# Kernel optimization log

Measured on AMD Instinct MI355X. Metric: run time of the kernel, lower is better.

Reference implementation:

```python
import jax, jax.numpy as jnp
import numpy as np

N, E, D, H = 100000, 200000, 384, 768
BN_EPS = 1e-5


def setup_inputs() -> dict:
    key = jax.random.key(0)
    ks = jax.random.split(key, 8)
    w = lambda k, sh: jax.random.normal(k, sh, jnp.float32) * 0.02
    return {
        "x": jax.random.normal(ks[0], (N, D), jnp.float32),
        "edge_attr": jax.random.normal(ks[1], (E, D), jnp.float32),
        "gamma": jnp.ones((D,), jnp.float32),
        "beta": jnp.zeros((D,), jnp.float32),
        "eps": jnp.zeros((), jnp.float32),          # GINE train_eps, init 0
        "W_edge": w(ks[2], (D, D)),
        "b_edge": jnp.zeros((D,), jnp.float32),
        "W1": w(ks[3], (D, H)),
        "b1": jnp.zeros((H,), jnp.float32),
        "W2": w(ks[4], (H, D)),
        "b2": jnp.zeros((D,), jnp.float32),
        "edge_index": jax.random.randint(ks[5], (2, E), 0, N, jnp.int32),
    }


def reference(x, edge_attr, gamma, beta, eps, W_edge, b_edge, W1, b1, W2, b2, edge_index):
    # BatchNorm1d over the node (batch) dimension, training statistics
    mu = jnp.mean(x, axis=0)
    var = jnp.var(x, axis=0)
    h = (x - mu) * jax.lax.rsqrt(var + BN_EPS) * gamma + beta  # [N, D]

    src, dst = edge_index[0], edge_index[1]  # j -> i (PyG source_to_target)
    # GINEConv message: relu(x_j + lin(edge_attr))
    msg = jax.nn.relu(h[src] + edge_attr @ W_edge + b_edge)     # [E, D]
    agg = jax.ops.segment_sum(msg, dst, num_segments=N)         # sum aggregation

    # nn((1+eps)*x_i + agg) where nn = Linear->GELU->Linear
    z = (1.0 + eps) * h + agg
    z = jax.nn.gelu(z @ W1 + b1, approximate=False) @ W2 + b2

    # residual + outer GELU activation (drop_path/dropout = identity at eval)
    return x + jax.nn.gelu(z, approximate=False)
```

## Files before the change

kernel.cpp:

```cpp
#include <hip/hip_runtime.h>
#include <hip/hip_bf16.h>

#define Df 384
#define Hf 768
#define SCAN_CH 4096

typedef __bf16 bf16x8 __attribute__((ext_vector_type(8)));
typedef float f32x4 __attribute__((ext_vector_type(4)));

struct __attribute__((aligned(4))) U12 { unsigned int x, y, z; };

__device__ inline unsigned short f2bf(float f) {
    __hip_bfloat16 h = __float2bfloat16(f);
    return __builtin_bit_cast(unsigned short, h);
}
__device__ inline float bf2f(unsigned short u) {
    unsigned int v = ((unsigned int)u) << 16;
    return __builtin_bit_cast(float, v);
}
__device__ inline float lobf(unsigned int v) { return bf2f((unsigned short)(v & 0xffff)); }
__device__ inline float hibf(unsigned int v) { return bf2f((unsigned short)(v >> 16)); }
__device__ inline unsigned int pk2(float a, float b) {
    return (unsigned int)f2bf(a) | ((unsigned int)f2bf(b) << 16);
}
__device__ inline float gelu_(float v) {
    return 0.5f * v * (1.0f + erff(v * 0.70710678118654752f));
}

__global__ void bn_stats(const float* __restrict__ x, float* __restrict__ stats, int N) {
    int t = threadIdx.x;
    int c4 = (t % 96) * 4;
    int rs = t / 96;
    float s0 = 0, s1 = 0, s2 = 0, s3 = 0, q0 = 0, q1 = 0, q2 = 0, q3 = 0;
    for (int r = blockIdx.x * 2 + rs; r < N; r += gridDim.x * 2) {
        float4 v = *(const float4*)(x + (size_t)r * Df + c4);
        s0 += v.x; s1 += v.y; s2 += v.z; s3 += v.w;
        q0 += v.x * v.x; q1 += v.y * v.y; q2 += v.z * v.z; q3 += v.w * v.w;
    }
    unsafeAtomicAdd(&stats[c4 + 0], s0);
    unsafeAtomicAdd(&stats[c4 + 1], s1);
    unsafeAtomicAdd(&stats[c4 + 2], s2);
    unsafeAtomicAdd(&stats[c4 + 3], s3);
    unsafeAtomicAdd(&stats[Df + c4 + 0], q0);
    unsafeAtomicAdd(&stats[Df + c4 + 1], q1);
    unsafeAtomicAdd(&stats[Df + c4 + 2], q2);
    unsafeAtomicAdd(&stats[Df + c4 + 3], q3);
}

__global__ void bn_finalize(const float* __restrict__ stats,
                            const float* __restrict__ gamma,
                            const float* __restrict__ beta,
                            float* __restrict__ coef, int N) {
    int c = threadIdx.x;
    float invN = 1.0f / (float)N;
    float mu = stats[c] * invN;
    float var = stats[Df + c] * invN - mu * mu;
    float rs = rsqrtf(var + 1e-5f);
    float a = gamma[c] * rs;
    coef[c] = a;
    coef[Df + c] = beta[c] - mu * a;
}

__global__ void h_kernel(const float* __restrict__ x, const float* __restrict__ coef,
                         unsigned short* __restrict__ hb, int tot8) {
    int i = blockIdx.x * 256 + threadIdx.x;
    if (i >= tot8) return;
    size_t base = (size_t)i * 8;
    int c = (int)(base % Df);
    float4 x0 = *(const float4*)(x + base);
    float4 x1 = *(const float4*)(x + base + 4);
    const float* a = coef + c;
    const float* b = coef + Df + c;
    uint4 o;
    o.x = pk2(x0.x * a[0] + b[0], x0.y * a[1] + b[1]);
    o.y = pk2(x0.z * a[2] + b[2], x0.w * a[3] + b[3]);
    o.z = pk2(x1.x * a[4] + b[4], x1.y * a[5] + b[5]);
    o.w = pk2(x1.z * a[6] + b[6], x1.w * a[7] + b[7]);
    *(uint4*)(hb + base) = o;
}

__global__ void wtrans(const float* __restrict__ Wsrc, unsigned short* __restrict__ Wdst,
                       int K, int Nc) {
    int idx = blockIdx.x * 256 + threadIdx.x;
    if (idx >= K * Nc) return;
    int k = idx / Nc, n = idx % Nc;
    Wdst[(size_t)n * K + k] = f2bf(Wsrc[idx]);
}

__global__ void degree_k(const int* __restrict__ dst, int* __restrict__ deg, int E) {
    int e = blockIdx.x * 256 + threadIdx.x;
    if (e < E) atomicAdd(&deg[dst[e]], 1);
}

__global__ void scan1(const int* __restrict__ deg, int* __restrict__ off,
                      int* __restrict__ sums, int N) {
    __shared__ int ts[256];
    int t = threadIdx.x;
    int base = blockIdx.x * SCAN_CH + t * 16;
    int v[16];
    int s = 0;
    for (int j = 0; j < 16; j++) {
        int idx = base + j;
        int d = (idx < N) ? deg[idx] : 0;
        v[j] = s;
        s += d;
    }
    ts[t] = s;
    __syncthreads();
    for (int o = 1; o < 256; o <<= 1) {
        int add = (t >= o) ? ts[t - o] : 0;
        __syncthreads();
        ts[t] += add;
        __syncthreads();
    }
    int pre = t ? ts[t - 1] : 0;
    for (int j = 0; j < 16; j++) {
        int idx = base + j;
        if (idx < N) off[idx] = pre + v[j];
    }
    if (t == 255) sums[blockIdx.x] = ts[255];
}

__global__ void scan2(int* __restrict__ sums, int nb) {
    int acc = 0;
    for (int b = 0; b < nb; b++) { int v = sums[b]; sums[b] = acc; acc += v; }
    sums[nb] = acc;
}

__global__ void scan3(int* __restrict__ off, const int* __restrict__ sums, int N, int nb) {
    int idx = blockIdx.x * 256 + threadIdx.x;
    if (idx < N) off[idx] += sums[idx / SCAN_CH];
    else if (idx == N) off[N] = sums[nb];
}

__global__ void fill_k(const int* __restrict__ dst, int* __restrict__ cursor,
                       int* __restrict__ eid, int E) {
    int e = blockIdx.x * 256 + threadIdx.x;
    if (e >= E) return;
    int pos = atomicAdd(&cursor[dst[e]], 1);
    eid[pos] = e;
}

__global__ __launch_bounds__(256) void aggregate(
    const unsigned short* __restrict__ msgl, const unsigned short* __restrict__ hb,
    const int* __restrict__ off, const int* __restrict__ eid,
    const int* __restrict__ edge_src, const float* __restrict__ epsp,
    unsigned short* __restrict__ zb, int N) {
    int lane = threadIdx.x & 63;
    int wid = threadIdx.x >> 6;
    int nwaves = gridDim.x * 4;
    float s1p = 1.0f + epsp[0];
    int loff = lane * 6;
    for (int i = blockIdx.x * 4 + wid; i < N; i += nwaves) {
        int o0 = off[i], o1 = off[i + 1];
        float a0 = 0, a1 = 0, a2 = 0, a3 = 0, a4 = 0, a5 = 0;
        for (int p = o0; p < o1; ++p) {
            int e = eid[p];
            int s = edge_src[e];
            U12 mv = *(const U12*)(msgl + (size_t)e * Df + loff);
            U12 hv = *(const U12*)(hb + (size_t)s * Df + loff);
            a0 += fmaxf(lobf(mv.x) + lobf(hv.x), 0.f);
            a1 += fmaxf(hibf(mv.x) + hibf(hv.x), 0.f);
            a2 += fmaxf(lobf(mv.y) + lobf(hv.y), 0.f);
            a3 += fmaxf(hibf(mv.y) + hibf(hv.y), 0.f);
            a4 += fmaxf(lobf(mv.z) + lobf(hv.z), 0.f);
            a5 += fmaxf(hibf(mv.z) + hibf(hv.z), 0.f);
        }
        U12 hv = *(const U12*)(hb + (size_t)i * Df + loff);
        U12 o;
        o.x = pk2(s1p * lobf(hv.x) + a0, s1p * hibf(hv.x) + a1);
        o.y = pk2(s1p * lobf(hv.y) + a2, s1p * hibf(hv.y) + a3);
        o.z = pk2(s1p * lobf(hv.z) + a4, s1p * hibf(hv.z) + a5);
        *(U12*)(zb + (size_t)i * Df + loff) = o;
    }
}

template <int EPI, bool ABF16>
__global__ __launch_bounds__(256) void gemm_fused(
    const void* __restrict__ Ap, const unsigned short* __restrict__ Bt,
    const float* __restrict__ bias, int M, int K,
    unsigned short* __restrict__ outb,
    const float* __restrict__ xres, float* __restrict__ outf, int ldo) {
    __shared__ unsigned short As[128][40];
    __shared__ unsigned short Bs[128][40];
    const int t = threadIdx.x;
    const int m0 = blockIdx.x * 128;
    const int n0 = blockIdx.y * 128;
    const int sr = t >> 1;
    const int sh = (t & 1) << 4;
    const int lane = t & 63;
    const int wid = t >> 6;
    const int wr = (wid >> 1) << 6;
    const int wc = (wid & 1) << 6;
    const int fr = lane & 15;
    const int kg = lane >> 4;

    f32x4 acc[4][4];
#pragma unroll
    for (int i = 0; i < 4; i++)
#pragma unroll
        for (int j = 0; j < 4; j++) acc[i][j] = (f32x4){0.f, 0.f, 0.f, 0.f};

    const bool arok = (m0 + sr) < M;
    const size_t arowoff = (size_t)(m0 + sr) * K;
    const unsigned short* Brow = Bt + (size_t)(n0 + sr) * K + sh;

    for (int k0 = 0; k0 < K; k0 += 32) {
        if (ABF16) {
            uint4 v0 = {0, 0, 0, 0}, v1 = {0, 0, 0, 0};
            if (arok) {
                const uint4* p = (const uint4*)((const unsigned short*)Ap + arowoff + k0 + sh);
                v0 = p[0]; v1 = p[1];
            }
            *(uint4*)&As[sr][sh] = v0;
            *(uint4*)&As[sr][sh + 8] = v1;
        } else {
            uint4 w0 = {0, 0, 0, 0}, w1 = {0, 0, 0, 0};
            if (arok) {
                const float4* p = (const float4*)((const float*)Ap + arowoff + k0 + sh);
                float4 f0 = p[0], f1 = p[1], f2 = p[2], f3 = p[3];
                w0.x = pk2(f0.x, f0.y); w0.y = pk2(f0.z, f0.w);
                w0.z = pk2(f1.x, f1.y); w0.w = pk2(f1.z, f1.w);
                w1.x = pk2(f2.x, f2.y); w1.y = pk2(f2.z, f2.w);
                w1.z = pk2(f3.x, f3.y); w1.w = pk2(f3.z, f3.w);
            }
            *(uint4*)&As[sr][sh] = w0;
            *(uint4*)&As[sr][sh + 8] = w1;
        }
        {
            const uint4* p = (const uint4*)(Brow + k0);
            *(uint4*)&Bs[sr][sh] = p[0];
            *(uint4*)&Bs[sr][sh + 8] = p[1];
        }
        __syncthreads();
        bf16x8 a[4], b[4];
#pragma unroll
        for (int i = 0; i < 4; i++) a[i] = *(const bf16x8*)&As[wr + i * 16 + fr][kg * 8];
#pragma unroll
        for (int j = 0; j < 4; j++) b[j] = *(const bf16x8*)&Bs[wc + j * 16 + fr][kg * 8];
#pragma unroll
        for (int i = 0; i < 4; i++)
#pragma unroll
            for (int j = 0; j < 4; j++)
                acc[i][j] = __builtin_amdgcn_mfma_f32_16x16x32_bf16(a[i], b[j], acc[i][j], 0, 0, 0);
        __syncthreads();
    }

    const int kg4 = kg * 4;
#pragma unroll
    for (int i = 0; i < 4; i++) {
        const int rb = m0 + wr + i * 16 + kg4;
#pragma unroll
        for (int j = 0; j < 4; j++) {
            const int c = n0 + wc + j * 16 + fr;
#pragma unroll
            for (int r = 0; r < 4; r++) {
                const int row = rb + r;
                if (row < M) {
                    float v = acc[i][j][r] + bias[c];
                    if (EPI == 1) {
                        outb[(size_t)row * ldo + c] = f2bf(gelu_(v));
                    } else if (EPI == 2) {
                        size_t o = (size_t)row * ldo + c;
                        outf[o] = xres[o] + gelu_(v);
                    } else {
                        outb[(size_t)row * ldo + c] = f2bf(v);
                    }
                }
            }
        }
    }
}

extern "C" void kernel_launch(void* const* d_in, const int* in_sizes, int n_in,
                              void* d_out, int out_size, void* d_ws, size_t ws_size,
                              hipStream_t stream) {
    const float* x = (const float*)d_in[0];
    const float* ea = (const float*)d_in[1];
    const float* gamma = (const float*)d_in[2];
    const float* beta = (const float*)d_in[3];
    const float* epsp = (const float*)d_in[4];
    const float* W_edge = (const float*)d_in[5];
    const float* b_edge = (const float*)d_in[6];
    const float* W1 = (const float*)d_in[7];
    const float* b1 = (const float*)d_in[8];
    const float* W2 = (const float*)d_in[9];
    const float* b2 = (const float*)d_in[10];
    const int* eidx = (const int*)d_in[11];
    float* out = (float*)d_out;
    const int N = in_sizes[0] / Df;
    const int E = in_sizes[1] / Df;
    const int* esrc = eidx;
    const int* edst = eidx + E;

    char* w = (char*)d_ws;
    size_t off_ = 0;
    auto alloc = [&](size_t bytes) { char* p = w + off_; off_ += (bytes + 255) & ~(size_t)255; return p; };
    float* stats = (float*)alloc(2 * Df * sizeof(float));
    float* coef = (float*)alloc(2 * Df * sizeof(float));
    unsigned short* hb = (unsigned short*)alloc((size_t)N * Df * 2);
    unsigned short* zb = (unsigned short*)alloc((size_t)N * Df * 2);
    unsigned short* tb = (unsigned short*)alloc((size_t)N * Hf * 2);
    unsigned short* WeT = (unsigned short*)alloc((size_t)Df * Df * 2);
    unsigned short* W1T = (unsigned short*)alloc((size_t)Df * Hf * 2);
    unsigned short* W2T = (unsigned short*)alloc((size_t)Hf * Df * 2);
    int* deg = (int*)alloc((size_t)(N + 1) * 4);
    int* offs = (int*)alloc((size_t)(N + 1) * 4);
    int* eid = (int*)alloc((size_t)E * 4);
    int* sums = (int*)alloc(64 * 4);
    size_t msgl_bytes = (size_t)E * Df * 2;
    unsigned short* msgl;
    if (off_ + msgl_bytes <= ws_size) msgl = (unsigned short*)alloc(msgl_bytes);
    else msgl = (unsigned short*)d_out;
    (void)n_in; (void)out_size;

    hipMemsetAsync(stats, 0, 2 * Df * sizeof(float), stream);
    hipMemsetAsync(deg, 0, (size_t)N * 4, stream);

    bn_stats<<<1024, 192, 0, stream>>>(x, stats, N);
    bn_finalize<<<1, Df, 0, stream>>>(stats, gamma, beta, coef, N);
    int tot8 = N * Df / 8;
    h_kernel<<<(tot8 + 255) / 256, 256, 0, stream>>>(x, coef, hb, tot8);

    wtrans<<<(Df * Df + 255) / 256, 256, 0, stream>>>(W_edge, WeT, Df, Df);
    wtrans<<<(Df * Hf + 255) / 256, 256, 0, stream>>>(W1, W1T, Df, Hf);
    wtrans<<<(Hf * Df + 255) / 256, 256, 0, stream>>>(W2, W2T, Hf, Df);

    int nb = (N + SCAN_CH - 1) / SCAN_CH;
    degree_k<<<(E + 255) / 256, 256, 0, stream>>>(edst, deg, E);
    scan1<<<nb, 256, 0, stream>>>(deg, offs, sums, N);
    scan2<<<1, 1, 0, stream>>>(sums, nb);
    scan3<<<(N + 256) / 256, 256, 0, stream>>>(offs, sums, N, nb);
    hipMemcpyAsync(deg, offs, (size_t)N * 4, hipMemcpyDeviceToDevice, stream);
    fill_k<<<(E + 255) / 256, 256, 0, stream>>>(edst, deg, eid, E);

    dim3 ge((E + 127) / 128, Df / 128);
    gemm_fused<3, false><<<ge, 256, 0, stream>>>(ea, WeT, b_edge, E, Df,
                                                 msgl, nullptr, nullptr, Df);

    aggregate<<<2048, 256, 0, stream>>>(msgl, hb, offs, eid, esrc, epsp, zb, N);

    dim3 g1((N + 127) / 128, Hf / 128);
    gemm_fused<1, true><<<g1, 256, 0, stream>>>(zb, W1T, b1, N, Df,
                                                tb, nullptr, nullptr, Hf);
    dim3 g2((N + 127) / 128, Df / 128);
    gemm_fused<2, true><<<g2, 256, 0, stream>>>(tb, W2T, b2, N, Hf,
                                                nullptr, x, out, Df);
}
```

Measured before the change: 1.188 ms.

## Write edge messages in dst-sorted order, use LDS direct loads, swap grid axes

The edge GEMM now scatters each message row to its CSR position (pose), and fill_k records the permuted source index. The aggregation then reads messages contiguously and drops the eid/edge_src double indirection. The GEMMs also load A (when bf16) and B tiles into unpadded LDS using global_load_lds, and the grid puts the N-tile index on the fast axis so blocks sharing an A row tile launch together. The cost is scattered row writes in the edge GEMM epilogue, and the unpadded LDS layout may cause bank conflicts on fragment reads.

New measurement: 1.114 ms. -6.3%, faster.

```diff
diff --git a/kernel.cpp b/kernel.cpp
--- a/kernel.cpp
+++ b/kernel.cpp
@@ -25,6 +25,11 @@
 }
 __device__ inline float gelu_(float v) {
     return 0.5f * v * (1.0f + erff(v * 0.70710678118654752f));
+}
+__device__ inline void gload16(const void* g, void* l) {
+    __builtin_amdgcn_global_load_lds(
+        (const __attribute__((address_space(1))) unsigned int*)g,
+        (__attribute__((address_space(3))) unsigned int*)l, 16, 0, 0);
 }
 
 __global__ void bn_stats(const float* __restrict__ x, float* __restrict__ stats, int N) {
@@ -133,18 +138,20 @@
     else if (idx == N) off[N] = sums[nb];
 }
 
-__global__ void fill_k(const int* __restrict__ dst, int* __restrict__ cursor,
-                       int* __restrict__ eid, int E) {
+__global__ void fill_k(const int* __restrict__ dst, const int* __restrict__ src,
+                       int* __restrict__ cursor, int* __restrict__ srcp,
+                       int* __restrict__ pose, int E) {
     int e = blockIdx.x * 256 + threadIdx.x;
     if (e >= E) return;
     int pos = atomicAdd(&cursor[dst[e]], 1);
-    eid[pos] = e;
+    srcp[pos] = src[e];
+    pose[e] = pos;
 }
 
 __global__ __launch_bounds__(256) void aggregate(
     const unsigned short* __restrict__ msgl, const unsigned short* __restrict__ hb,
-    const int* __restrict__ off, const int* __restrict__ eid,
-    const int* __restrict__ edge_src, const float* __restrict__ epsp,
+    const int* __restrict__ off, const int* __restrict__ srcp,
+    const float* __restrict__ epsp,
     unsigned short* __restrict__ zb, int N) {
     int lane = threadIdx.x & 63;
     int wid = threadIdx.x >> 6;
@@ -155,9 +162,8 @@
         int o0 = off[i], o1 = off[i + 1];
         float a0 = 0, a1 = 0, a2 = 0, a3 = 0, a4 = 0, a5 = 0;
         for (int p = o0; p < o1; ++p) {
-            int e = eid[p];
-            int s = edge_src[e];
-            U12 mv = *(const U12*)(msgl + (size_t)e * Df + loff);
+            int s = srcp[p];
+            U12 mv = *(const U12*)(msgl + (size_t)p * Df + loff);
             U12 hv = *(const U12*)(hb + (size_t)s * Df + loff);
             a0 += fmaxf(lobf(mv.x) + lobf(hv.x), 0.f);
             a1 += fmaxf(hibf(mv.x) + hibf(hv.x), 0.f);
@@ -179,21 +185,24 @@
 __global__ __launch_bounds__(256) void gemm_fused(
     const void* __restrict__ Ap, const unsigned short* __restrict__ Bt,
     const float* __restrict__ bias, int M, int K,
+    const int* __restrict__ pose,
     unsigned short* __restrict__ outb,
     const float* __restrict__ xres, float* __restrict__ outf, int ldo) {
-    __shared__ unsigned short As[128][40];
-    __shared__ unsigned short Bs[128][40];
+    __shared__ __align__(16) unsigned short As[128 * 32];
+    __shared__ __align__(16) unsigned short Bs[128 * 32];
     const int t = threadIdx.x;
-    const int m0 = blockIdx.x * 128;
-    const int n0 = blockIdx.y * 128;
-    const int sr = t >> 1;
-    const int sh = (t & 1) << 4;
+    const int n0 = blockIdx.x * 128;
+    const int m0 = blockIdx.y * 128;
     const int lane = t & 63;
     const int wid = t >> 6;
     const int wr = (wid >> 1) << 6;
     const int wc = (wid & 1) << 6;
     const int fr = lane & 15;
     const int kg = lane >> 4;
+    const int crow = lane >> 2;
+    const int cseg = lane & 3;
+    const int sr = t >> 1;
+    const int sh = (t & 1) << 4;
 
     f32x4 acc[4][4];
 #pragma unroll
@@ -203,17 +212,17 @@
 
     const bool arok = (m0 + sr) < M;
     const size_t arowoff = (size_t)(m0 + sr) * K;
-    const unsigned short* Brow = Bt + (size_t)(n0 + sr) * K + sh;
 
     for (int k0 = 0; k0 < K; k0 += 32) {
         if (ABF16) {
-            uint4 v0 = {0, 0, 0, 0}, v1 = {0, 0, 0, 0};
-            if (arok) {
-                const uint4* p = (const uint4*)((const unsigned short*)Ap + arowoff + k0 + sh);
-                v0 = p[0]; v1 = p[1];
+            const unsigned short* Ab = (const unsigned short*)Ap;
+#pragma unroll
+            for (int c = 0; c < 2; c++) {
+                const int row = wid * 32 + c * 16 + crow;
+                if (m0 + row < M)
+                    gload16(Ab + (size_t)(m0 + row) * K + k0 + cseg * 8,
+                            &As[(wid * 32 + c * 16) * 32]);
             }
-            *(uint4*)&As[sr][sh] = v0;
-            *(uint4*)&As[sr][sh + 8] = v1;
         } else {
             uint4 w0 = {0, 0, 0, 0}, w1 = {0, 0, 0, 0};
             if (arok) {
@@ -224,20 +233,21 @@
                 w1.x = pk2(f2.x, f2.y); w1.y = pk2(f2.z, f2.w);
                 w1.z = pk2(f3.x, f3.y); w1.w = pk2(f3.z, f3.w);
             }
-            *(uint4*)&As[sr][sh] = w0;
-            *(uint4*)&As[sr][sh + 8] = w1;
+            *(uint4*)&As[sr * 32 + sh] = w0;
+            *(uint4*)&As[sr * 32 + sh + 8] = w1;
         }
-        {
-            const uint4* p = (const uint4*)(Brow + k0);
-            *(uint4*)&Bs[sr][sh] = p[0];
-            *(uint4*)&Bs[sr][sh + 8] = p[1];
+#pragma unroll
+        for (int c = 0; c < 2; c++) {
+            const int row = wid * 32 + c * 16 + crow;
+            gload16(Bt + (size_t)(n0 + row) * K + k0 + cseg * 8,
+                    &Bs[(wid * 32 + c * 16) * 32]);
         }
         __syncthreads();
         bf16x8 a[4], b[4];
 #pragma unroll
-        for (int i = 0; i < 4; i++) a[i] = *(const bf16x8*)&As[wr + i * 16 + fr][kg * 8];
-#pragma unroll
-        for (int j = 0; j < 4; j++) b[j] = *(const bf16x8*)&Bs[wc + j * 16 + fr][kg * 8];
+        for (int i = 0; i < 4; i++) a[i] = *(const bf16x8*)&As[(wr + i * 16 + fr) * 32 + kg * 8];
+#pragma unroll
+        for (int j = 0; j < 4; j++) b[j] = *(const bf16x8*)&Bs[(wc + j * 16 + fr) * 32 + kg * 8];
 #pragma unroll
         for (int i = 0; i < 4; i++)
 #pragma unroll
@@ -264,7 +274,7 @@
                         size_t o = (size_t)row * ldo + c;
                         outf[o] = xres[o] + gelu_(v);
                     } else {
-                        outb[(size_t)row * ldo + c] = f2bf(v);
+                        outb[(size_t)pose[row] * ldo + c] = f2bf(v);
                     }
                 }
             }
@@ -306,7 +316,8 @@
     unsigned short* W2T = (unsigned short*)alloc((size_t)Hf * Df * 2);
     int* deg = (int*)alloc((size_t)(N + 1) * 4);
     int* offs = (int*)alloc((size_t)(N + 1) * 4);
-    int* eid = (int*)alloc((size_t)E * 4);
+    int* srcp = (int*)alloc((size_t)E * 4);
+    int* pose = (int*)alloc((size_t)E * 4);
     int* sums = (int*)alloc(64 * 4);
     size_t msgl_bytes = (size_t)E * Df * 2;
     unsigned short* msgl;
@@ -332,18 +343,18 @@
     scan2<<<1, 1, 0, stream>>>(sums, nb);
     scan3<<<(N + 256) / 256, 256, 0, stream>>>(offs, sums, N, nb);
     hipMemcpyAsync(deg, offs, (size_t)N * 4, hipMemcpyDeviceToDevice, stream);
-    fill_k<<<(E + 255) / 256, 256, 0, stream>>>(edst, deg, eid, E);
-
-    dim3 ge((E + 127) / 128, Df / 128);
+    fill_k<<<(E + 255) / 256, 256, 0, stream>>>(edst, esrc, deg, srcp, pose, E);
+
+    dim3 ge(Df / 128, (E + 127) / 128);
     gemm_fused<3, false><<<ge, 256, 0, stream>>>(ea, WeT, b_edge, E, Df,
-                                                 msgl, nullptr, nullptr, Df);
-
-    aggregate<<<2048, 256, 0, stream>>>(msgl, hb, offs, eid, esrc, epsp, zb, N);
-
-    dim3 g1((N + 127) / 128, Hf / 128);
+                                                 pose, msgl, nullptr, nullptr, Df);
+
+    aggregate<<<2048, 256, 0, stream>>>(msgl, hb, offs, srcp, epsp, zb, N);
+
+    dim3 g1(Hf / 128, (N + 127) / 128);
     gemm_fused<1, true><<<g1, 256, 0, stream>>>(zb, W1T, b1, N, Df,
-                                                tb, nullptr, nullptr, Hf);
-    dim3 g2((N + 127) / 128, Df / 128);
+                                                nullptr, tb, nullptr, nullptr, Hf);
+    dim3 g2(Df / 128, (N + 127) / 128);
     gemm_fused<2, true><<<g2, 256, 0, stream>>>(tb, W2T, b2, N, Hf,
-                                                nullptr, x, out, Df);
-}
+                                                nullptr, nullptr, x, out, Df);
+}
```
